# Kernel tuning notes

Measured on AMD Instinct MI355X. Metric: run time of the kernel, lower is better.

Reference implementation:

```python
import jax, jax.numpy as jnp
import numpy as np
import math

CHUNK = 33554432  # 2**25, power of two so the 2^n index space is fully covered


def setup_inputs() -> dict:
    key = jax.random.key(0)
    k1, k2 = jax.random.split(key)
    phi_vals = jax.random.normal(k1, (CHUNK,), dtype=jnp.float32)
    weights = jax.random.uniform(k2, (CHUNK,), dtype=jnp.float32)
    return {"phi_vals": phi_vals, "weights": weights}


def reference(phi_vals, weights):
    # Analytic closed form of the PennyLane circuit:
    #   n index qubits in uniform superposition, Hadamard-sandwiched ancilla h,
    #   per-index controlled-RZ(2*w_p*phi_p) on a |0> target kicks phase
    #   e^{-i w_p phi_p} onto the h=1 branch of index state p.
    #   <Z_h> = (sum_p cos(w_p * phi_p) + (2^n - C)) / 2^n
    C = phi_vals.shape[0]
    n = int(math.ceil(math.log2(C)))
    N = 2 ** n
    s = jnp.sum(jnp.cos(weights * phi_vals))
    return (s + jnp.float32(N - C)) / jnp.float32(N)
```

## Files before the change

kernel.cpp:

```cpp
#include <hip/hip_runtime.h>


#define RBLOCKS 2048
#define RTHREADS 256

typedef float v4f __attribute__((ext_vector_type(4)));

__global__ __launch_bounds__(RTHREADS) void qs_partial_kernel(
    const float* __restrict__ phi, const float* __restrict__ w,
    float* __restrict__ partials, int n4, int n) {
    const v4f* __restrict__ p4 = (const v4f*)phi;
    const v4f* __restrict__ w4 = (const v4f*)w;

    const int span  = (n4 + (int)gridDim.x - 1) / (int)gridDim.x;
    const int start = (int)blockIdx.x * span;
    const int lim   = (start + span < n4) ? (start + span) : n4;

    float acc0 = 0.0f, acc1 = 0.0f, acc2 = 0.0f, acc3 = 0.0f;
    int i = start + (int)threadIdx.x;

    for (; i + 3 * RTHREADS < lim; i += 4 * RTHREADS) {
        v4f a0 = __builtin_nontemporal_load(p4 + i);
        v4f a1 = __builtin_nontemporal_load(p4 + i + RTHREADS);
        v4f a2 = __builtin_nontemporal_load(p4 + i + 2 * RTHREADS);
        v4f a3 = __builtin_nontemporal_load(p4 + i + 3 * RTHREADS);
        v4f b0 = __builtin_nontemporal_load(w4 + i);
        v4f b1 = __builtin_nontemporal_load(w4 + i + RTHREADS);
        v4f b2 = __builtin_nontemporal_load(w4 + i + 2 * RTHREADS);
        v4f b3 = __builtin_nontemporal_load(w4 + i + 3 * RTHREADS);
        acc0 += __cosf(a0.x * b0.x) + __cosf(a0.y * b0.y)
              + __cosf(a0.z * b0.z) + __cosf(a0.w * b0.w);
        acc1 += __cosf(a1.x * b1.x) + __cosf(a1.y * b1.y)
              + __cosf(a1.z * b1.z) + __cosf(a1.w * b1.w);
        acc2 += __cosf(a2.x * b2.x) + __cosf(a2.y * b2.y)
              + __cosf(a2.z * b2.z) + __cosf(a2.w * b2.w);
        acc3 += __cosf(a3.x * b3.x) + __cosf(a3.y * b3.y)
              + __cosf(a3.z * b3.z) + __cosf(a3.w * b3.w);
    }
    for (; i < lim; i += RTHREADS) {
        v4f a = __builtin_nontemporal_load(p4 + i);
        v4f b = __builtin_nontemporal_load(w4 + i);
        acc0 += __cosf(a.x * b.x) + __cosf(a.y * b.y)
              + __cosf(a.z * b.z) + __cosf(a.w * b.w);
    }
    if (blockIdx.x == 0 && threadIdx.x == 0) {
        for (int j = n4 * 4; j < n; ++j) acc0 += __cosf(phi[j] * w[j]);
    }

    float acc = (acc0 + acc1) + (acc2 + acc3);

    #pragma unroll
    for (int off = 32; off > 0; off >>= 1)
        acc += __shfl_down(acc, off, 64);

    __shared__ float smem[RTHREADS / 64];
    int lane = threadIdx.x & 63;
    int wid  = threadIdx.x >> 6;
    if (lane == 0) smem[wid] = acc;
    __syncthreads();
    if (threadIdx.x == 0) {
        float t = 0.0f;
        #pragma unroll
        for (int k = 0; k < RTHREADS / 64; ++k) t += smem[k];
        partials[blockIdx.x] = t;
    }
}

__global__ __launch_bounds__(1024) void qs_final_kernel(
    const float* __restrict__ partials, float* __restrict__ out,
    int nb, float addend, float inv_n) {
    float acc = 0.0f;
    for (int i = threadIdx.x; i < nb; i += blockDim.x) acc += partials[i];

    #pragma unroll
    for (int off = 32; off > 0; off >>= 1)
        acc += __shfl_down(acc, off, 64);

    __shared__ float smem[1024 / 64];
    int lane = threadIdx.x & 63;
    int wid  = threadIdx.x >> 6;
    if (lane == 0) smem[wid] = acc;
    __syncthreads();
    if (threadIdx.x == 0) {
        float t = 0.0f;
        #pragma unroll
        for (int k = 0; k < 1024 / 64; ++k) t += smem[k];
        out[0] = (t + addend) * inv_n;
    }
}

extern "C" void kernel_launch(void* const* d_in, const int* in_sizes, int n_in,
                              void* d_out, int out_size, void* d_ws, size_t ws_size,
                              hipStream_t stream) {
    const float* phi = (const float*)d_in[0];
    const float* w   = (const float*)d_in[1];
    float* out       = (float*)d_out;
    float* partials  = (float*)d_ws;

    int n  = in_sizes[0];
    int n4 = n >> 2;

    long long N = 1;
    while (N < (long long)n) N <<= 1;
    float addend = (float)(N - (long long)n);
    float inv_n  = 1.0f / (float)N;

    qs_partial_kernel<<<RBLOCKS, RTHREADS, 0, stream>>>(phi, w, partials, n4, n);
    qs_final_kernel<<<1, 1024, 0, stream>>>(partials, out, RBLOCKS, addend, inv_n);
}
```

Measured before the change: 247.3 us.

## Split reduction into two kernels, using system-scope nontemporal loads for last eighth

Divides the input so the first seven eighths go through the existing vectorized partial kernel on 1792 blocks. The last eighth goes through a second kernel on 256 blocks that issues inline-asm global_load_dwordx4 with sc0 sc1 nt cache bits and an explicit waitcnt. The aim appears to be pulling data through a different cache path, possibly bypassing the MALL/L2 state. The cost is an extra kernel launch, serialized after the first on the same stream, and a less pipelined loop in the second kernel.

```diff
diff --git a/kernel.cpp b/kernel.cpp
--- a/kernel.cpp
+++ b/kernel.cpp
@@ -1,20 +1,44 @@
 #include <hip/hip_runtime.h>
 
 
-#define RBLOCKS 2048
 #define RTHREADS 256
+#define ABLOCKS 1792
+#define BBLOCKS 256
 
 typedef float v4f __attribute__((ext_vector_type(4)));
 
+__device__ __forceinline__ float cos4(v4f a, v4f b) {
+    return __cosf(a.x * b.x) + __cosf(a.y * b.y)
+         + __cosf(a.z * b.z) + __cosf(a.w * b.w);
+}
+
+__device__ __forceinline__ void block_reduce_store(
+    float acc, float* __restrict__ dst) {
+    #pragma unroll
+    for (int off = 32; off > 0; off >>= 1)
+        acc += __shfl_down(acc, off, 64);
+    __shared__ float smem[RTHREADS / 64];
+    int lane = threadIdx.x & 63;
+    int wid  = threadIdx.x >> 6;
+    if (lane == 0) smem[wid] = acc;
+    __syncthreads();
+    if (threadIdx.x == 0) {
+        float t = 0.0f;
+        #pragma unroll
+        for (int k = 0; k < RTHREADS / 64; ++k) t += smem[k];
+        *dst = t;
+    }
+}
+
 __global__ __launch_bounds__(RTHREADS) void qs_partial_kernel(
     const float* __restrict__ phi, const float* __restrict__ w,
-    float* __restrict__ partials, int n4, int n) {
+    float* __restrict__ partials, int lim4, int n4, int n) {
     const v4f* __restrict__ p4 = (const v4f*)phi;
     const v4f* __restrict__ w4 = (const v4f*)w;
 
-    const int span  = (n4 + (int)gridDim.x - 1) / (int)gridDim.x;
+    const int span  = (lim4 + (int)gridDim.x - 1) / (int)gridDim.x;
     const int start = (int)blockIdx.x * span;
-    const int lim   = (start + span < n4) ? (start + span) : n4;
+    const int lim   = (start + span < lim4) ? (start + span) : lim4;
 
     float acc0 = 0.0f, acc1 = 0.0f, acc2 = 0.0f, acc3 = 0.0f;
     int i = start + (int)threadIdx.x;
@@ -28,42 +52,63 @@
         v4f b1 = __builtin_nontemporal_load(w4 + i + RTHREADS);
         v4f b2 = __builtin_nontemporal_load(w4 + i + 2 * RTHREADS);
         v4f b3 = __builtin_nontemporal_load(w4 + i + 3 * RTHREADS);
-        acc0 += __cosf(a0.x * b0.x) + __cosf(a0.y * b0.y)
-              + __cosf(a0.z * b0.z) + __cosf(a0.w * b0.w);
-        acc1 += __cosf(a1.x * b1.x) + __cosf(a1.y * b1.y)
-              + __cosf(a1.z * b1.z) + __cosf(a1.w * b1.w);
-        acc2 += __cosf(a2.x * b2.x) + __cosf(a2.y * b2.y)
-              + __cosf(a2.z * b2.z) + __cosf(a2.w * b2.w);
-        acc3 += __cosf(a3.x * b3.x) + __cosf(a3.y * b3.y)
-              + __cosf(a3.z * b3.z) + __cosf(a3.w * b3.w);
+        acc0 += cos4(a0, b0);
+        acc1 += cos4(a1, b1);
+        acc2 += cos4(a2, b2);
+        acc3 += cos4(a3, b3);
     }
     for (; i < lim; i += RTHREADS) {
         v4f a = __builtin_nontemporal_load(p4 + i);
         v4f b = __builtin_nontemporal_load(w4 + i);
-        acc0 += __cosf(a.x * b.x) + __cosf(a.y * b.y)
-              + __cosf(a.z * b.z) + __cosf(a.w * b.w);
+        acc0 += cos4(a, b);
     }
     if (blockIdx.x == 0 && threadIdx.x == 0) {
         for (int j = n4 * 4; j < n; ++j) acc0 += __cosf(phi[j] * w[j]);
     }
 
-    float acc = (acc0 + acc1) + (acc2 + acc3);
+    block_reduce_store((acc0 + acc1) + (acc2 + acc3),
+                       &partials[blockIdx.x]);
+}
 
-    #pragma unroll
-    for (int off = 32; off > 0; off >>= 1)
-        acc += __shfl_down(acc, off, 64);
+__device__ __forceinline__ v4f ld_sys_nt(const v4f* p) {
+    v4f r;
+    asm volatile("global_load_dwordx4 %0, %1, off sc0 sc1 nt"
+                 : "=&v"(r) : "v"(p));
+    return r;
+}
 
-    __shared__ float smem[RTHREADS / 64];
-    int lane = threadIdx.x & 63;
-    int wid  = threadIdx.x >> 6;
-    if (lane == 0) smem[wid] = acc;
-    __syncthreads();
-    if (threadIdx.x == 0) {
-        float t = 0.0f;
-        #pragma unroll
-        for (int k = 0; k < RTHREADS / 64; ++k) t += smem[k];
-        partials[blockIdx.x] = t;
+__global__ __launch_bounds__(RTHREADS) void qs_partial_sys_kernel(
+    const float* __restrict__ phi, const float* __restrict__ w,
+    float* __restrict__ partials, int start4, int n4) {
+    const v4f* __restrict__ p4 = (const v4f*)phi;
+    const v4f* __restrict__ w4 = (const v4f*)w;
+
+    const int len   = n4 - start4;
+    const int span  = (len + (int)gridDim.x - 1) / (int)gridDim.x;
+    const int start = start4 + (int)blockIdx.x * span;
+    const int lim   = (start + span < n4) ? (start + span) : n4;
+
+    float acc0 = 0.0f, acc1 = 0.0f;
+    int i = start + (int)threadIdx.x;
+
+    for (; i + RTHREADS < lim; i += 2 * RTHREADS) {
+        v4f a0 = ld_sys_nt(p4 + i);
+        v4f a1 = ld_sys_nt(p4 + i + RTHREADS);
+        v4f b0 = ld_sys_nt(w4 + i);
+        v4f b1 = ld_sys_nt(w4 + i + RTHREADS);
+        asm volatile("s_waitcnt vmcnt(0)"
+                     : "+v"(a0), "+v"(a1), "+v"(b0), "+v"(b1));
+        __builtin_amdgcn_sched_barrier(0);
+        acc0 += cos4(a0, b0);
+        acc1 += cos4(a1, b1);
     }
+    for (; i < lim; i += RTHREADS) {
+        v4f a = __builtin_nontemporal_load(p4 + i);
+        v4f b = __builtin_nontemporal_load(w4 + i);
+        acc0 += cos4(a, b);
+    }
+
+    block_reduce_store(acc0 + acc1, &partials[blockIdx.x]);
 }
 
 __global__ __launch_bounds__(1024) void qs_final_kernel(
@@ -100,11 +145,17 @@
     int n  = in_sizes[0];
     int n4 = n >> 2;
 
+    int split = (int)(((long long)n4 * 7) / 8);
+
     long long N = 1;
     while (N < (long long)n) N <<= 1;
     float addend = (float)(N - (long long)n);
     float inv_n  = 1.0f / (float)N;
 
-    qs_partial_kernel<<<RBLOCKS, RTHREADS, 0, stream>>>(phi, w, partials, n4, n);
-    qs_final_kernel<<<1, 1024, 0, stream>>>(partials, out, RBLOCKS, addend, inv_n);
+    qs_partial_kernel<<<ABLOCKS, RTHREADS, 0, stream>>>(
+        phi, w, partials, split, n4, n);
+    qs_partial_sys_kernel<<<BBLOCKS, RTHREADS, 0, stream>>>(
+        phi, w, partials + ABLOCKS, split, n4);
+    qs_final_kernel<<<1, 1024, 0, stream>>>(
+        partials, out, ABLOCKS + BBLOCKS, addend, inv_n);
 }
```

Result: no change. 251.1 us (+1.5%).
